# Kernel tuning notes

Hardware: AMD Instinct MI355X
Metric: run time of the kernel (lower is better)

## Reference

```python
import jax, jax.numpy as jnp
import numpy as np
from jax import lax

NUM_HEADS = 6
LN_EPS = 1e-5


def _ln(x, g, b):
    mu = jnp.mean(x, axis=-1, keepdims=True)
    var = jnp.mean(jnp.square(x - mu), axis=-1, keepdims=True)
    return (x - mu) * jax.lax.rsqrt(var + LN_EPS) * g + b


def _gelu(x):
    return jax.nn.gelu(x, approximate=False)


def setup_inputs() -> dict:
    key = jax.random.key(0)
    ks = jax.random.split(key, 16)
    B, N, C = 16, 1025, 384
    hid = 4 * C  # 1536
    k3 = 3  # depthwise kernel size
    s = 0.02
    rn = lambda k, shape: (jax.random.normal(k, shape, jnp.float32) * s)
    return {
        "x": jax.random.normal(ks[0], (B, N, C), jnp.float32),
        "ln1_g": jnp.ones((C,), jnp.float32),
        "ln1_b": jnp.zeros((C,), jnp.float32),
        "qkv_w": rn(ks[1], (3 * C, C)),
        "proj_w": rn(ks[2], (C, C)),
        "proj_b": jnp.zeros((C,), jnp.float32),
        "ln2_g": jnp.ones((C,), jnp.float32),
        "ln2_b": jnp.zeros((C,), jnp.float32),
        "conv1_w": rn(ks[3], (hid, C)),          # 1x1 conv as matrix
        "conv1_b": jnp.zeros((hid,), jnp.float32),
        "conv2_w": rn(ks[4], (hid, 1, k3, k3)),   # depthwise OIHW
        "conv2_b": jnp.zeros((hid,), jnp.float32),
        "conv3_w": rn(ks[5], (C, hid)),           # 1x1 conv as matrix
        "conv3_b": jnp.zeros((C,), jnp.float32),
        "bn1_s": jnp.ones((hid,), jnp.float32), "bn1_b": jnp.zeros((hid,), jnp.float32),
        "bn2_s": jnp.ones((hid,), jnp.float32), "bn2_b": jnp.zeros((hid,), jnp.float32),
        "bn3_s": jnp.ones((C,), jnp.float32), "bn3_b": jnp.zeros((C,), jnp.float32),
        "comp_w": rn(ks[6], (C // 4, C)), "comp_b": jnp.zeros((C // 4,), jnp.float32),
        "exc_w": rn(ks[7], (C, C // 4)), "exc_b": jnp.zeros((C,), jnp.float32),
    }


def _block(x, ln1_g, ln1_b, qkv_w, proj_w, proj_b, ln2_g, ln2_b,
           conv1_w, conv1_b, conv2_w, conv2_b, conv3_w, conv3_b,
           bn1_s, bn1_b, bn2_s, bn2_b, bn3_s, bn3_b,
           comp_w, comp_b, exc_w, exc_b):
    B, N, C = x.shape
    Hh = NUM_HEADS
    hd = C // Hh
    S = int(np.sqrt(N - 1))

    # ---- Attention (manual softmax(QK^T)V) ----
    h = _ln(x, ln1_g, ln1_b)
    qkv = jnp.einsum('bnc,dc->bnd', h, qkv_w).reshape(B, N, 3, Hh, hd)
    qkv = qkv.transpose(2, 0, 3, 1, 4)  # [3,B,H,N,hd]
    q, k, v = qkv[0], qkv[1], qkv[2]
    attn = jax.nn.softmax(jnp.einsum('bhqd,bhkd->bhqk', q, k) * (hd ** -0.5), axis=-1)
    o = jnp.einsum('bhqk,bhkd->bhqd', attn, v).transpose(0, 2, 1, 3).reshape(B, N, C)
    o = o @ proj_w.T + proj_b
    x = x + o

    # ---- DAFF FFN (conv + BN(eval affine) + GELU + SE gating on cls) ----
    h2 = _ln(x, ln2_g, ln2_b)
    cls_tok, tok = h2[:, :1], h2[:, 1:]
    t = tok.reshape(B, S, S, C).transpose(0, 3, 1, 2)  # NCHW
    hid = conv1_w.shape[0]
    y = jnp.einsum('bchw,oc->bohw', t, conv1_w) + conv1_b[None, :, None, None]
    y = y * bn1_s[None, :, None, None] + bn1_b[None, :, None, None]
    y = _gelu(y)
    shortcut = y
    y = lax.conv_general_dilated(y, conv2_w, (1, 1), 'SAME',
                                 feature_group_count=hid,
                                 dimension_numbers=('NCHW', 'OIHW', 'NCHW'))
    y = y + conv2_b[None, :, None, None]
    y = y * bn2_s[None, :, None, None] + bn2_b[None, :, None, None]
    y = shortcut + _gelu(y)
    y = jnp.einsum('bchw,oc->bohw', y, conv3_w) + conv3_b[None, :, None, None]
    y = y * bn3_s[None, :, None, None] + bn3_b[None, :, None, None]
    # SE gate on cls token
    w = jnp.mean(y, axis=(2, 3)).reshape(B, 1, C)
    w = _gelu(w @ comp_w.T + comp_b) @ exc_w.T + exc_b
    cls_out = cls_tok * w
    tok_out = y.reshape(B, C, S * S).transpose(0, 2, 1)
    out = jnp.concatenate([cls_out, tok_out], axis=1)
    return x + out


def reference(x, ln1_g, ln1_b, qkv_w, proj_w, proj_b, ln2_g, ln2_b,
              conv1_w, conv1_b, conv2_w, conv2_b, conv3_w, conv3_b,
              bn1_s, bn1_b, bn2_s, bn2_b, bn3_s, bn3_b,
              comp_w, comp_b, exc_w, exc_b):
    return _block(x, ln1_g, ln1_b, qkv_w, proj_w, proj_b, ln2_g, ln2_b,
                  conv1_w, conv1_b, conv2_w, conv2_b, conv3_w, conv3_b,
                  bn1_s, bn1_b, bn2_s, bn2_b, bn3_s, bn3_b,
                  comp_w, comp_b, exc_w, exc_b)
```

## Files before the change

kernel.cpp:

```cpp
#include <hip/hip_runtime.h>
#include <math.h>

#define DI __device__ __forceinline__

namespace {

constexpr int B_ = 16;
constexpr int N_ = 1025;
constexpr int C_ = 384;
constexpr int H_ = 6;
constexpr int HD_ = 64;
constexpr int HID_ = 1536;
constexpr int P_ = 1024;
constexpr int MTOK = B_ * P_;
constexpr int MALL = B_ * N_;
constexpr int NPAD = 1088;
constexpr long long AF = (long long)MALL * C_;

typedef __attribute__((ext_vector_type(4))) float f32x4;
typedef __attribute__((ext_vector_type(8))) short bf16x8;

DI float gelu_f(float x) { return 0.5f * x * (1.0f + erff(x * 0.7071067811865475f)); }

DI float us2f(unsigned short u) {
  union { unsigned int i; float f; } c; c.i = ((unsigned)u) << 16; return c.f;
}
DI unsigned short f2us(float f) {
  union { float f; unsigned int i; } c; c.f = f;
  unsigned int r = c.i + 0x7FFF + ((c.i >> 16) & 1);
  return (unsigned short)(r >> 16);
}
DI unsigned short f2us_trunc(float f) {
  union { float f; unsigned int i; } c; c.f = f;
  return (unsigned short)(c.i >> 16);
}
DI void bf8_to_f(const uint4 v, float* f) {
  const unsigned int u[4] = {v.x, v.y, v.z, v.w};
#pragma unroll
  for (int t = 0; t < 4; t++) {
    union { unsigned int i; float fl; } lo, hi;
    lo.i = (u[t] & 0xffffu) << 16;
    hi.i = u[t] & 0xffff0000u;
    f[2 * t] = lo.fl; f[2 * t + 1] = hi.fl;
  }
}
DI uint4 f_to_bf8(const float* f) {
  unsigned int w[4];
#pragma unroll
  for (int t = 0; t < 4; t++)
    w[t] = (unsigned)f2us(f[2 * t]) | ((unsigned)f2us(f[2 * t + 1]) << 16);
  return make_uint4(w[0], w[1], w[2], w[3]);
}

DI void gl2lds16(const unsigned short* g, unsigned short* l) {
  __builtin_amdgcn_global_load_lds(
      (const __attribute__((address_space(1))) void*)g,
      (__attribute__((address_space(3))) void*)l, 16, 0, 0);
}

__global__ __launch_bounds__(256) void cvt_kernel(const float* __restrict__ src,
                                                  unsigned short* __restrict__ dst, int n)
{
  const int i = blockIdx.x * 256 + threadIdx.x;
  if (i < n) dst[i] = f2us(src[i]);
}

__global__ __launch_bounds__(256) void wprep_kernel(
    const float* __restrict__ w2, const float* __restrict__ c2b,
    const float* __restrict__ s2, const float* __restrict__ b2,
    unsigned short* __restrict__ w2s, float* __restrict__ Bc)
{
  const int idx = blockIdx.x * 256 + threadIdx.x;
  if (idx < HID_ * 9) {
    const int tap = idx / HID_, c = idx % HID_;
    w2s[tap * HID_ + c] = f2us(w2[c * 9 + tap] * s2[c]);
  }
  if (idx < HID_) Bc[idx] = c2b[idx] * s2[idx] + b2[idx];
}

__global__ __launch_bounds__(128) void ln_kernel(
    const float* __restrict__ x, const float* __restrict__ g,
    const float* __restrict__ b, unsigned short* __restrict__ out,
    float* __restrict__ cls_out)
{
  const int row = blockIdx.x;
  const int t = threadIdx.x;
  const float* xr = x + (long long)row * C_;
  float v0 = xr[t], v1 = xr[t + 128], v2 = xr[t + 256];
  __shared__ float rs[128], rq[128];
  rs[t] = v0 + v1 + v2;
  rq[t] = v0 * v0 + v1 * v1 + v2 * v2;
  __syncthreads();
  for (int o = 64; o > 0; o >>= 1) {
    if (t < o) { rs[t] += rs[t + o]; rq[t] += rq[t + o]; }
    __syncthreads();
  }
  const float mean = rs[0] * (1.0f / C_);
  const float var  = rq[0] * (1.0f / C_) - mean * mean;
  const float rstd = rsqrtf(var + 1e-5f);
  unsigned short* orow = out + (long long)row * C_;
  const float r0 = (v0 - mean) * rstd * g[t]       + b[t];
  const float r1 = (v1 - mean) * rstd * g[t + 128] + b[t + 128];
  const float r2 = (v2 - mean) * rstd * g[t + 256] + b[t + 256];
  orow[t] = f2us(r0); orow[t + 128] = f2us(r1); orow[t + 256] = f2us(r2);
  if (cls_out != nullptr && (row % N_) == 0) {
    const int bb = row / N_;
    float* cr = cls_out + (long long)bb * C_;
    cr[t] = r0; cr[t + 128] = r1; cr[t + 256] = r2;
  }
}

__global__ __launch_bounds__(256) void vtrans_kernel(
    const unsigned short* __restrict__ v, unsigned short* __restrict__ vt)
{
  __shared__ unsigned short t[64][72];
  const int bh = blockIdx.x, nt = blockIdx.y;
  const int n0 = nt * 64;
  const int tid = threadIdx.x;
  {
    const int nl = tid >> 2;
    const int dc = (tid & 3) * 16;
    const int gn = n0 + nl;
    uint4 a = make_uint4(0u,0u,0u,0u), b = make_uint4(0u,0u,0u,0u);
    if (gn < N_) {
      const unsigned short* p = v + ((long long)bh * N_ + gn) * HD_ + dc;
      a = *(const uint4*)p; b = *(const uint4*)(p + 8);
    }
    *(uint4*)&t[nl][dc] = a;
    *(uint4*)&t[nl][dc + 8] = b;
  }
  __syncthreads();
  {
    const int dl = tid >> 2;
    const int nc = (tid & 3) * 16;
    unsigned short tmp[16];
#pragma unroll
    for (int i = 0; i < 16; i++) tmp[i] = t[nc + i][dl];
    unsigned short* p = vt + ((long long)bh * HD_ + dl) * NPAD + n0 + nc;
    *(uint4*)p = *(uint4*)&tmp[0];
    *(uint4*)(p + 8) = *(uint4*)&tmp[8];
  }
}

enum { GM_QKV = 0, GM_PROJ = 1, GM_CONV1 = 2, GM_CONV3 = 3 };

template <int MODE, int K>
__global__ __launch_bounds__(256) void mgemm_kernel(
    const unsigned short* __restrict__ A, const unsigned short* __restrict__ W,
    void* __restrict__ o0, void* __restrict__ o1, void* __restrict__ o2,
    const float* __restrict__ e0, const float* __restrict__ e1,
    const float* __restrict__ e2, int M)
{
  __shared__ unsigned short As[128][64];
  __shared__ unsigned short Bs[128][64];
  const int m0 = blockIdx.x * 128, n0 = blockIdx.y * 128;
  if (m0 >= M) return;
  const int tid = threadIdx.x;
  const int lane = tid & 63, wv = tid >> 6;
  const int lane15 = lane & 15, quad = lane >> 4;
  const int wm = (wv >> 1) * 64, wn = (wv & 1) * 64;

  const unsigned short* agp[4];
  const unsigned short* bgp[4];
#pragma unroll
  for (int t = 0; t < 4; t++) {
    const int lr = wv * 32 + t * 8 + (lane >> 3);
    const int chunk = (lane & 7) ^ (lr & 7);
    int gm = m0 + lr;
    if (gm > M - 1) gm = M - 1;
    long long arow = gm;
    if constexpr (MODE == GM_CONV1) arow = (long long)(gm >> 10) * N_ + 1 + (gm & 1023);
    agp[t] = A + arow * K + chunk * 8;
    bgp[t] = W + (long long)(n0 + lr) * K + chunk * 8;
  }

  f32x4 acc[4][4];
#pragma unroll
  for (int i = 0; i < 4; i++)
#pragma unroll
    for (int j = 0; j < 4; j++) acc[i][j] = (f32x4)0.f;

  const int xsel = lane15 & 7;
  for (int k0 = 0; k0 < K; k0 += 64) {
    __syncthreads();
#pragma unroll
    for (int t = 0; t < 4; t++) {
      gl2lds16(agp[t] + k0, &As[wv * 32 + t * 8][0]);
      gl2lds16(bgp[t] + k0, &Bs[wv * 32 + t * 8][0]);
    }
    __syncthreads();
#pragma unroll
    for (int kh = 0; kh < 2; kh++) {
      bf16x8 af[4], bfr[4];
#pragma unroll
      for (int i = 0; i < 4; i++)
        af[i] = *(const bf16x8*)&As[wm + i * 16 + lane15][((kh * 4 + quad) ^ xsel) * 8];
#pragma unroll
      for (int j = 0; j < 4; j++)
        bfr[j] = *(const bf16x8*)&Bs[wn + j * 16 + lane15][((kh * 4 + quad) ^ xsel) * 8];
#pragma unroll
      for (int i = 0; i < 4; i++)
#pragma unroll
        for (int j = 0; j < 4; j++)
          acc[i][j] = __builtin_amdgcn_mfma_f32_16x16x32_bf16(af[i], bfr[j], acc[i][j], 0, 0, 0);
    }
  }
#pragma unroll
  for (int i = 0; i < 4; i++) {
#pragma unroll
    for (int r = 0; r < 4; r++) {
      const int m = m0 + wm + i * 16 + quad * 4 + r;
      if (m >= M) continue;
#pragma unroll
      for (int j = 0; j < 4; j++) {
        const int n = n0 + wn + j * 16 + lane15;
        const float val = acc[i][j][r];
        if constexpr (MODE == GM_QKV) {
          const int which = n / C_, rr = n % C_, hh = rr >> 6, e = rr & 63;
          const int b = m / N_, nn = m % N_;
          unsigned short* dst = (unsigned short*)((which == 0) ? o0 : ((which == 1) ? o1 : o2));
          const float sval = (which == 0) ? val * 0.125f : val;
          dst[(((long long)b * H_ + hh) * N_ + nn) * HD_ + e] = f2us(sval);
        } else if constexpr (MODE == GM_PROJ) {
          ((float*)o0)[(long long)m * C_ + n] = val + e0[(long long)m * C_ + n] + e1[n];
        } else if constexpr (MODE == GM_CONV1) {
          ((unsigned short*)o0)[(long long)m * HID_ + n] =
              f2us(gelu_f((val + e0[n]) * e1[n] + e2[n]));
        } else {
          ((float*)o0)[(long long)m * C_ + n] = (val + e0[n]) * e1[n] + e2[n];
        }
      }
    }
  }
}

__global__ __launch_bounds__(256) void fattn_kernel(
    const unsigned short* __restrict__ q, const unsigned short* __restrict__ k,
    const unsigned short* __restrict__ vt, unsigned short* __restrict__ o)
{
  __shared__ unsigned short Ks[64][64];
  __shared__ unsigned short Vt[64][64];
  __shared__ unsigned short Ps[4][16][72];
  const int tid = threadIdx.x;
  const int lane = tid & 63, wv = tid >> 6;
  const int lane15 = lane & 15, quad = lane >> 4;
  const int bh = blockIdx.x, qt = blockIdx.y;
  const long long headoff = (long long)bh * N_;
  const int q0 = qt * 64 + wv * 16;

  const long long qrow = headoff + q0 + lane15;
  const bf16x8 aq0 = *(const bf16x8*)(q + qrow * HD_ + quad * 8);
  const bf16x8 aq1 = *(const bf16x8*)(q + qrow * HD_ + 32 + quad * 8);

  const unsigned short* kgp[2];
  const unsigned short* vgp[2];
#pragma unroll
  for (int t = 0; t < 2; t++) {
    const int row = wv * 16 + t * 8 + (lane >> 3);
    const int ch = (lane & 7) ^ (row & 7);
    kgp[t] = k + (headoff + row) * HD_ + ch * 8;
    vgp[t] = vt + ((long long)bh * HD_ + row) * NPAD + ch * 8;
  }

  f32x4 O[4];
  float l_r[4] = {0.f, 0.f, 0.f, 0.f};
#pragma unroll
  for (int n = 0; n < 4; n++) O[n] = (f32x4)0.f;

  const int xsel = lane15 & 7;
  for (int kt = 0; kt < 17; kt++) {
    const int kt0 = kt * 64;
    __syncthreads();
#pragma unroll
    for (int t = 0; t < 2; t++) {
      gl2lds16(kgp[t] + (long long)kt0 * HD_, &Ks[wv * 16 + t * 8][0]);
      gl2lds16(vgp[t] + kt0, &Vt[wv * 16 + t * 8][0]);
    }
    __syncthreads();

    f32x4 S[4];
#pragma unroll
    for (int n = 0; n < 4; n++) {
      S[n] = (f32x4)0.f;
      const bf16x8 b0 = *(const bf16x8*)&Ks[n * 16 + lane15][(quad ^ xsel) * 8];
      S[n] = __builtin_amdgcn_mfma_f32_16x16x32_bf16(aq0, b0, S[n], 0, 0, 0);
      const bf16x8 b1 = *(const bf16x8*)&Ks[n * 16 + lane15][((4 + quad) ^ xsel) * 8];
      S[n] = __builtin_amdgcn_mfma_f32_16x16x32_bf16(aq1, b1, S[n], 0, 0, 0);
    }
    if (kt == 16) {
#pragma unroll
      for (int n = 0; n < 4; n++) {
        if ((kt0 + n * 16 + lane15) >= N_)
#pragma unroll
          for (int r = 0; r < 4; r++) S[n][r] = -1e30f;
      }
    }
#pragma unroll
    for (int n = 0; n < 4; n++)
#pragma unroll
      for (int r = 0; r < 4; r++) {
        const float p = __expf(S[n][r]);
        l_r[r] += p;
        Ps[wv][quad * 4 + r][n * 16 + lane15] = f2us_trunc(p);
      }
#pragma unroll
    for (int half = 0; half < 2; half++) {
      const bf16x8 ap = *(const bf16x8*)&Ps[wv][lane15][half * 32 + quad * 8];
#pragma unroll
      for (int n = 0; n < 4; n++) {
        const bf16x8 bv =
            *(const bf16x8*)&Vt[n * 16 + lane15][(((half * 4 + quad)) ^ xsel) * 8];
        O[n] = __builtin_amdgcn_mfma_f32_16x16x32_bf16(ap, bv, O[n], 0, 0, 0);
      }
    }
  }
#pragma unroll
  for (int msk = 1; msk < 16; msk <<= 1)
#pragma unroll
    for (int r = 0; r < 4; r++) l_r[r] += __shfl_xor(l_r[r], msk, 64);

  const int b = bh / H_, hh = bh % H_;
#pragma unroll
  for (int r = 0; r < 4; r++) {
    const int gq = q0 + quad * 4 + r;
    if (gq < N_) {
      const float inv = 1.0f / l_r[r];
#pragma unroll
      for (int n = 0; n < 4; n++)
        o[((long long)b * N_ + gq) * C_ + hh * HD_ + n * 16 + lane15] = f2us(O[n][r] * inv);
    }
  }
}

__global__ __launch_bounds__(192) void dwconv_kernel(
    const unsigned short* __restrict__ y1, const unsigned short* __restrict__ w2s,
    const float* __restrict__ Bc, unsigned short* __restrict__ y2)
{
  const int p = blockIdx.x & 1023;
  const int b = blockIdx.x >> 10;
  const int i = p >> 5, j = p & 31;
  const int cb = threadIdx.x << 3;
  const long long tokbase = (long long)blockIdx.x * HID_;
  float acc[8] = {};
#pragma unroll
  for (int di = -1; di <= 1; di++) {
    const int ii = i + di;
    if (ii < 0 || ii > 31) continue;
#pragma unroll
    for (int dj = -1; dj <= 1; dj++) {
      const int jj = j + dj;
      if (jj < 0 || jj > 31) continue;
      const int tap = (di + 1) * 3 + (dj + 1);
      const uint4 dv = *(const uint4*)(y1 + ((long long)b * P_ + ii * 32 + jj) * HID_ + cb);
      const uint4 wv = *(const uint4*)(w2s + tap * HID_ + cb);
      float df[8], wf[8];
      bf8_to_f(dv, df); bf8_to_f(wv, wf);
#pragma unroll
      for (int t = 0; t < 8; t++) acc[t] += df[t] * wf[t];
    }
  }
  const uint4 sv = *(const uint4*)(y1 + tokbase + cb);
  float sf[8]; bf8_to_f(sv, sf);
  const float4 bc0 = *(const float4*)(Bc + cb);
  const float4 bc1 = *(const float4*)(Bc + cb + 4);
  const float bcv[8] = {bc0.x, bc0.y, bc0.z, bc0.w, bc1.x, bc1.y, bc1.z, bc1.w};
  float of[8];
#pragma unroll
  for (int t = 0; t < 8; t++) of[t] = sf[t] + gelu_f(acc[t] + bcv[t]);
  *(uint4*)(y2 + tokbase + cb) = f_to_bf8(of);
}

__global__ __launch_bounds__(384) void pool_kernel(const float* __restrict__ y3,
                                                   float* __restrict__ w0p)
{
  const int b = blockIdx.x, chunk = blockIdx.y;
  const int c = threadIdx.x;
  float s = 0.f;
  for (int p = chunk * 64; p < chunk * 64 + 64; p++)
    s += y3[((long long)b * P_ + p) * C_ + c];
  w0p[((long long)b * 16 + chunk) * C_ + c] = s;
}

__global__ __launch_bounds__(128) void se_kernel(
    const float* __restrict__ w0p, const float* __restrict__ cw,
    const float* __restrict__ cb, const float* __restrict__ ew,
    const float* __restrict__ eb, float* __restrict__ wfin)
{
  __shared__ float wm[384];
  __shared__ float t1[96];
  const int b = blockIdx.x, t = threadIdx.x;
  for (int c = t; c < 384; c += 128) {
    float s = 0.f;
    for (int ch = 0; ch < 16; ch++) s += w0p[((long long)b * 16 + ch) * C_ + c];
    wm[c] = s * (1.0f / 1024.0f);
  }
  __syncthreads();
  if (t < 96) {
    float s = cb[t];
    for (int c = 0; c < 384; c++) s += wm[c] * cw[t * 384 + c];
    t1[t] = gelu_f(s);
  }
  __syncthreads();
  for (int c = t; c < 384; c += 128) {
    float s = eb[c];
    for (int j = 0; j < 96; j++) s += t1[j] * ew[c * 96 + j];
    wfin[(long long)b * C_ + c] = s;
  }
}

__global__ __launch_bounds__(256) void assemble_kernel(
    const float* __restrict__ x2, const float* __restrict__ cls,
    const float* __restrict__ y3, const float* __restrict__ wfin,
    float* __restrict__ out)
{
  const long long idx = (long long)blockIdx.x * 256 + threadIdx.x;
  if (idx >= AF) return;
  const int c = (int)(idx % C_);
  const long long row = idx / C_;
  const int b = (int)(row / N_);
  const int n = (int)(row % N_);
  float add;
  if (n == 0) add = cls[(long long)b * C_ + c] * wfin[(long long)b * C_ + c];
  else        add = y3[((long long)b * P_ + n - 1) * C_ + c];
  out[idx] = x2[idx] + add;
}

}

extern "C" void kernel_launch(void* const* d_in, const int* in_sizes, int n_in,
                              void* d_out, int out_size, void* d_ws, size_t ws_size,
                              hipStream_t stream)
{
  const float* x       = (const float*)d_in[0];
  const float* ln1_g   = (const float*)d_in[1];
  const float* ln1_b   = (const float*)d_in[2];
  const float* qkv_w   = (const float*)d_in[3];
  const float* proj_w  = (const float*)d_in[4];
  const float* proj_b  = (const float*)d_in[5];
  const float* ln2_g   = (const float*)d_in[6];
  const float* ln2_b   = (const float*)d_in[7];
  const float* conv1_w = (const float*)d_in[8];
  const float* conv1_b = (const float*)d_in[9];
  const float* conv2_w = (const float*)d_in[10];
  const float* conv2_b = (const float*)d_in[11];
  const float* conv3_w = (const float*)d_in[12];
  const float* conv3_b = (const float*)d_in[13];
  const float* bn1_s   = (const float*)d_in[14];
  const float* bn1_b   = (const float*)d_in[15];
  const float* bn2_s   = (const float*)d_in[16];
  const float* bn2_b   = (const float*)d_in[17];
  const float* bn3_s   = (const float*)d_in[18];
  const float* bn3_b   = (const float*)d_in[19];
  const float* comp_w  = (const float*)d_in[20];
  const float* comp_b  = (const float*)d_in[21];
  const float* exc_w   = (const float*)d_in[22];
  const float* exc_b   = (const float*)d_in[23];

  char* wsb = (char*)d_ws;
  const size_t RA = 50331648, RB = 50331648, RC = 25190400;
  const int NQKV = 3 * C_ * C_;
  const int NPROJ = C_ * C_;
  const int NC1 = HID_ * C_;
  const int NC3 = C_ * HID_;
  const int NW2 = HID_ * 9;
  const size_t tailbytes = (size_t)(NQKV + NPROJ + NC1 + NC3 + NW2) * 2 +
                           (size_t)(HID_ + B_ * C_ + B_ * 16 * C_ + B_ * C_) * 4;
  const size_t needed = RA + RB + RC + tailbytes;
  if (ws_size < needed) return;

  unsigned short* qb  = (unsigned short*)wsb;
  unsigned short* kb  = qb + AF;
  unsigned short* vb  = kb + AF;
  unsigned short* h2b = (unsigned short*)wsb;
  unsigned short* y2  = (unsigned short*)wsb;
  char* rb = wsb + RA;
  unsigned short* hb  = (unsigned short*)rb;
  unsigned short* o16 = (unsigned short*)rb;
  unsigned short* y1  = (unsigned short*)rb;
  float* y3           = (float*)rb;
  unsigned short* vtb = (unsigned short*)(wsb + RA + RB);
  float* x2 = (float*)(wsb + RA + RB);
  unsigned short* wqkv16 = (unsigned short*)(wsb + RA + RB + RC);
  unsigned short* wproj16 = wqkv16 + NQKV;
  unsigned short* wc116 = wproj16 + NPROJ;
  unsigned short* wc316 = wc116 + NC1;
  unsigned short* w2s  = wc316 + NC3;
  float* Bc   = (float*)(w2s + NW2);
  float* cls  = Bc + HID_;
  float* w0p  = cls + B_ * C_;
  float* wfin = w0p + B_ * 16 * C_;

  cvt_kernel<<<(NQKV + 255) / 256, 256, 0, stream>>>(qkv_w, wqkv16, NQKV);
  cvt_kernel<<<(NPROJ + 255) / 256, 256, 0, stream>>>(proj_w, wproj16, NPROJ);
  cvt_kernel<<<(NC1 + 255) / 256, 256, 0, stream>>>(conv1_w, wc116, NC1);
  cvt_kernel<<<(NC3 + 255) / 256, 256, 0, stream>>>(conv3_w, wc316, NC3);
  wprep_kernel<<<(NW2 + 255) / 256, 256, 0, stream>>>(conv2_w, conv2_b, bn2_s, bn2_b, w2s, Bc);
  ln_kernel<<<MALL, 128, 0, stream>>>(x, ln1_g, ln1_b, hb, nullptr);
  mgemm_kernel<GM_QKV, 384><<<dim3(136, 9), 256, 0, stream>>>(
      hb, wqkv16, qb, kb, vb, nullptr, nullptr, nullptr, MALL);
  vtrans_kernel<<<dim3(B_ * H_, 17), 256, 0, stream>>>(vb, vtb);
  fattn_kernel<<<dim3(B_ * H_, 17), 256, 0, stream>>>(qb, kb, vtb, o16);
  mgemm_kernel<GM_PROJ, 384><<<dim3(136, 3), 256, 0, stream>>>(
      o16, wproj16, x2, nullptr, nullptr, x, proj_b, nullptr, MALL);
  ln_kernel<<<MALL, 128, 0, stream>>>(x2, ln2_g, ln2_b, h2b, cls);
  mgemm_kernel<GM_CONV1, 384><<<dim3(128, 12), 256, 0, stream>>>(
      h2b, wc116, y1, nullptr, nullptr, conv1_b, bn1_s, bn1_b, MTOK);
  dwconv_kernel<<<MTOK, 192, 0, stream>>>(y1, w2s, Bc, y2);
  mgemm_kernel<GM_CONV3, 1536><<<dim3(128, 3), 256, 0, stream>>>(
      y2, wc316, y3, nullptr, nullptr, conv3_b, bn3_s, bn3_b, MTOK);
  pool_kernel<<<dim3(B_, 16), 384, 0, stream>>>(y3, w0p);
  se_kernel<<<B_, 128, 0, stream>>>(w0p, comp_w, comp_b, exc_w, exc_b, wfin);
  assemble_kernel<<<(int)((AF + 255) / 256), 256, 0, stream>>>(x2, cls, y3, wfin, (float*)d_out);
}
```

Baseline: 442.5 us.

## Fuse residual into conv3 epilogue, warp-level LN, exp2 softmax, 2-token dwconv

Merges weight conversion kernels into one launch and rewrites LayerNorm to use one wavefront per row with shuffle reductions. Folds log2(e) into the Q scale so attention can use exp2. Processes two adjacent tokens per depthwise-conv block to reuse loaded columns and weights. Moves the final residual add into the conv3 GEMM epilogue, leaving only a small cls-row fix kernel, which removes a full-tensor pass at the cost of scattered epilogue writes.

```diff
diff --git a/kernel.cpp b/kernel.cpp
--- a/kernel.cpp
+++ b/kernel.cpp
@@ -17,6 +17,14 @@
 constexpr int NPAD = 1088;
 constexpr long long AF = (long long)MALL * C_;
 
+constexpr int NQKV = 3 * C_ * C_;
+constexpr int NPROJ = C_ * C_;
+constexpr int NC1 = HID_ * C_;
+constexpr int NC3 = C_ * HID_;
+constexpr int NW2 = HID_ * 9;
+constexpr int T1 = NQKV, T2 = T1 + NPROJ, T3 = T2 + NC1, T4 = T3 + NC3;
+constexpr int T5 = T4 + NW2, T6 = T5 + HID_;
+
 typedef __attribute__((ext_vector_type(4))) float f32x4;
 typedef __attribute__((ext_vector_type(8))) short bf16x8;
 
@@ -58,55 +66,59 @@
       (__attribute__((address_space(3))) void*)l, 16, 0, 0);
 }
 
-__global__ __launch_bounds__(256) void cvt_kernel(const float* __restrict__ src,
-                                                  unsigned short* __restrict__ dst, int n)
-{
-  const int i = blockIdx.x * 256 + threadIdx.x;
-  if (i < n) dst[i] = f2us(src[i]);
-}
-
-__global__ __launch_bounds__(256) void wprep_kernel(
-    const float* __restrict__ w2, const float* __restrict__ c2b,
+__global__ __launch_bounds__(256) void cvtall_kernel(
+    const float* __restrict__ qkv_w, const float* __restrict__ proj_w,
+    const float* __restrict__ conv1_w, const float* __restrict__ conv3_w,
+    const float* __restrict__ conv2_w, const float* __restrict__ c2b,
     const float* __restrict__ s2, const float* __restrict__ b2,
-    unsigned short* __restrict__ w2s, float* __restrict__ Bc)
+    unsigned short* __restrict__ dst16, float* __restrict__ Bc)
 {
   const int idx = blockIdx.x * 256 + threadIdx.x;
-  if (idx < HID_ * 9) {
-    const int tap = idx / HID_, c = idx % HID_;
-    w2s[tap * HID_ + c] = f2us(w2[c * 9 + tap] * s2[c]);
-  }
-  if (idx < HID_) Bc[idx] = c2b[idx] * s2[idx] + b2[idx];
-}
-
-__global__ __launch_bounds__(128) void ln_kernel(
+  if (idx < T1)      dst16[idx] = f2us(qkv_w[idx]);
+  else if (idx < T2) dst16[idx] = f2us(proj_w[idx - T1]);
+  else if (idx < T3) dst16[idx] = f2us(conv1_w[idx - T2]);
+  else if (idx < T4) dst16[idx] = f2us(conv3_w[idx - T3]);
+  else if (idx < T5) {
+    const int r = idx - T4, tap = r / HID_, c = r % HID_;
+    dst16[idx] = f2us(conv2_w[c * 9 + tap] * s2[c]);
+  } else if (idx < T6) {
+    const int c = idx - T5;
+    Bc[c] = c2b[c] * s2[c] + b2[c];
+  }
+}
+
+__global__ __launch_bounds__(256) void lnw_kernel(
     const float* __restrict__ x, const float* __restrict__ g,
     const float* __restrict__ b, unsigned short* __restrict__ out,
-    float* __restrict__ cls_out)
-{
-  const int row = blockIdx.x;
-  const int t = threadIdx.x;
+    float* __restrict__ cls_out, int nrows)
+{
+  const int row = blockIdx.x * 4 + (threadIdx.x >> 6);
+  if (row >= nrows) return;
+  const int lane = threadIdx.x & 63;
   const float* xr = x + (long long)row * C_;
-  float v0 = xr[t], v1 = xr[t + 128], v2 = xr[t + 256];
-  __shared__ float rs[128], rq[128];
-  rs[t] = v0 + v1 + v2;
-  rq[t] = v0 * v0 + v1 * v1 + v2 * v2;
-  __syncthreads();
-  for (int o = 64; o > 0; o >>= 1) {
-    if (t < o) { rs[t] += rs[t + o]; rq[t] += rq[t + o]; }
-    __syncthreads();
-  }
-  const float mean = rs[0] * (1.0f / C_);
-  const float var  = rq[0] * (1.0f / C_) - mean * mean;
+  float v[6];
+#pragma unroll
+  for (int i = 0; i < 6; i++) v[i] = xr[lane + 64 * i];
+  float s = 0.f, q = 0.f;
+#pragma unroll
+  for (int i = 0; i < 6; i++) { s += v[i]; q += v[i] * v[i]; }
+#pragma unroll
+  for (int m = 1; m < 64; m <<= 1) {
+    s += __shfl_xor(s, m, 64);
+    q += __shfl_xor(q, m, 64);
+  }
+  const float mean = s * (1.0f / C_);
+  const float var  = q * (1.0f / C_) - mean * mean;
   const float rstd = rsqrtf(var + 1e-5f);
   unsigned short* orow = out + (long long)row * C_;
-  const float r0 = (v0 - mean) * rstd * g[t]       + b[t];
-  const float r1 = (v1 - mean) * rstd * g[t + 128] + b[t + 128];
-  const float r2 = (v2 - mean) * rstd * g[t + 256] + b[t + 256];
-  orow[t] = f2us(r0); orow[t + 128] = f2us(r1); orow[t + 256] = f2us(r2);
-  if (cls_out != nullptr && (row % N_) == 0) {
-    const int bb = row / N_;
-    float* cr = cls_out + (long long)bb * C_;
-    cr[t] = r0; cr[t + 128] = r1; cr[t + 256] = r2;
+  const bool iscls = (cls_out != nullptr) && (row % N_) == 0;
+  float* cr = iscls ? cls_out + (long long)(row / N_) * C_ : nullptr;
+#pragma unroll
+  for (int i = 0; i < 6; i++) {
+    const int c = lane + 64 * i;
+    const float r = (v[i] - mean) * rstd * g[c] + b[c];
+    orow[c] = f2us(r);
+    if (iscls) cr[c] = r;
   }
 }
 
@@ -219,7 +231,7 @@
           const int which = n / C_, rr = n % C_, hh = rr >> 6, e = rr & 63;
           const int b = m / N_, nn = m % N_;
           unsigned short* dst = (unsigned short*)((which == 0) ? o0 : ((which == 1) ? o1 : o2));
-          const float sval = (which == 0) ? val * 0.125f : val;
+          const float sval = (which == 0) ? val * 0.18033688f : val;
           dst[(((long long)b * H_ + hh) * N_ + nn) * HD_ + e] = f2us(sval);
         } else if constexpr (MODE == GM_PROJ) {
           ((float*)o0)[(long long)m * C_ + n] = val + e0[(long long)m * C_ + n] + e1[n];
@@ -227,7 +239,11 @@
           ((unsigned short*)o0)[(long long)m * HID_ + n] =
               f2us(gelu_f((val + e0[n]) * e1[n] + e2[n]));
         } else {
-          ((float*)o0)[(long long)m * C_ + n] = (val + e0[n]) * e1[n] + e2[n];
+          const float val2 = (val + e0[n]) * e1[n] + e2[n];
+          ((float*)o0)[(long long)m * C_ + n] = val2;
+          const int bb = m >> 10, pp = m & 1023;
+          const long long orow = ((long long)bb * N_ + 1 + pp) * C_ + n;
+          ((float*)o1)[orow] = ((const float*)o2)[orow] + val2;
         }
       }
     }
@@ -299,7 +315,7 @@
     for (int n = 0; n < 4; n++)
 #pragma unroll
       for (int r = 0; r < 4; r++) {
-        const float p = __expf(S[n][r]);
+        const float p = exp2f(S[n][r]);
         l_r[r] += p;
         Ps[wv][quad * 4 + r][n * 16 + lane15] = f2us_trunc(p);
       }
@@ -336,38 +352,63 @@
     const unsigned short* __restrict__ y1, const unsigned short* __restrict__ w2s,
     const float* __restrict__ Bc, unsigned short* __restrict__ y2)
 {
-  const int p = blockIdx.x & 1023;
-  const int b = blockIdx.x >> 10;
-  const int i = p >> 5, j = p & 31;
+  const int jp = blockIdx.x & 15;
+  const int i  = (blockIdx.x >> 4) & 31;
+  const int b  = blockIdx.x >> 9;
+  const int j0 = jp * 2;
   const int cb = threadIdx.x << 3;
-  const long long tokbase = (long long)blockIdx.x * HID_;
-  float acc[8] = {};
+
+  float wf[9][8];
+#pragma unroll
+  for (int tap = 0; tap < 9; tap++) {
+    const uint4 wv = *(const uint4*)(w2s + tap * HID_ + cb);
+    bf8_to_f(wv, wf[tap]);
+  }
+  float acc0[8] = {}, acc1[8] = {};
+  float sh0[8], sh1[8];
 #pragma unroll
   for (int di = -1; di <= 1; di++) {
     const int ii = i + di;
     if (ii < 0 || ii > 31) continue;
-#pragma unroll
-    for (int dj = -1; dj <= 1; dj++) {
-      const int jj = j + dj;
+    const long long rowbase = ((long long)b * P_ + ii * 32) * HID_ + cb;
+#pragma unroll
+    for (int dj = -1; dj <= 2; dj++) {
+      const int jj = j0 + dj;
       if (jj < 0 || jj > 31) continue;
-      const int tap = (di + 1) * 3 + (dj + 1);
-      const uint4 dv = *(const uint4*)(y1 + ((long long)b * P_ + ii * 32 + jj) * HID_ + cb);
-      const uint4 wv = *(const uint4*)(w2s + tap * HID_ + cb);
-      float df[8], wf[8];
-      bf8_to_f(dv, df); bf8_to_f(wv, wf);
-#pragma unroll
-      for (int t = 0; t < 8; t++) acc[t] += df[t] * wf[t];
-    }
-  }
-  const uint4 sv = *(const uint4*)(y1 + tokbase + cb);
-  float sf[8]; bf8_to_f(sv, sf);
+      const uint4 dv = *(const uint4*)(y1 + rowbase + (long long)jj * HID_);
+      float df[8]; bf8_to_f(dv, df);
+      if (dj <= 1) {
+        const int tap = (di + 1) * 3 + (dj + 1);
+#pragma unroll
+        for (int t = 0; t < 8; t++) acc0[t] += df[t] * wf[tap][t];
+      }
+      if (dj >= 0) {
+        const int tap = (di + 1) * 3 + dj;
+#pragma unroll
+        for (int t = 0; t < 8; t++) acc1[t] += df[t] * wf[tap][t];
+      }
+      if (di == 0 && dj == 0) {
+#pragma unroll
+        for (int t = 0; t < 8; t++) sh0[t] = df[t];
+      }
+      if (di == 0 && dj == 1) {
+#pragma unroll
+        for (int t = 0; t < 8; t++) sh1[t] = df[t];
+      }
+    }
+  }
   const float4 bc0 = *(const float4*)(Bc + cb);
   const float4 bc1 = *(const float4*)(Bc + cb + 4);
   const float bcv[8] = {bc0.x, bc0.y, bc0.z, bc0.w, bc1.x, bc1.y, bc1.z, bc1.w};
-  float of[8];
-#pragma unroll
-  for (int t = 0; t < 8; t++) of[t] = sf[t] + gelu_f(acc[t] + bcv[t]);
-  *(uint4*)(y2 + tokbase + cb) = f_to_bf8(of);
+  float of0[8], of1[8];
+#pragma unroll
+  for (int t = 0; t < 8; t++) {
+    of0[t] = sh0[t] + gelu_f(acc0[t] + bcv[t]);
+    of1[t] = sh1[t] + gelu_f(acc1[t] + bcv[t]);
+  }
+  const long long tok0 = ((long long)b * P_ + i * 32 + j0) * HID_ + cb;
+  *(uint4*)(y2 + tok0) = f_to_bf8(of0);
+  *(uint4*)(y2 + tok0 + HID_) = f_to_bf8(of1);
 }
 
 __global__ __launch_bounds__(384) void pool_kernel(const float* __restrict__ y3,
@@ -408,21 +449,15 @@
   }
 }
 
-__global__ __launch_bounds__(256) void assemble_kernel(
+__global__ __launch_bounds__(256) void clsfix_kernel(
     const float* __restrict__ x2, const float* __restrict__ cls,
-    const float* __restrict__ y3, const float* __restrict__ wfin,
-    float* __restrict__ out)
-{
-  const long long idx = (long long)blockIdx.x * 256 + threadIdx.x;
-  if (idx >= AF) return;
-  const int c = (int)(idx % C_);
-  const long long row = idx / C_;
-  const int b = (int)(row / N_);
-  const int n = (int)(row % N_);
-  float add;
-  if (n == 0) add = cls[(long long)b * C_ + c] * wfin[(long long)b * C_ + c];
-  else        add = y3[((long long)b * P_ + n - 1) * C_ + c];
-  out[idx] = x2[idx] + add;
+    const float* __restrict__ wfin, float* __restrict__ out)
+{
+  const int idx = blockIdx.x * 256 + threadIdx.x;
+  if (idx >= B_ * C_) return;
+  const int b = idx / C_, c = idx % C_;
+  const long long row = (long long)b * N_ * C_ + c;
+  out[row] = x2[row] + cls[idx] * wfin[idx];
 }
 
 }
@@ -458,12 +493,7 @@
 
   char* wsb = (char*)d_ws;
   const size_t RA = 50331648, RB = 50331648, RC = 25190400;
-  const int NQKV = 3 * C_ * C_;
-  const int NPROJ = C_ * C_;
-  const int NC1 = HID_ * C_;
-  const int NC3 = C_ * HID_;
-  const int NW2 = HID_ * 9;
-  const size_t tailbytes = (size_t)(NQKV + NPROJ + NC1 + NC3 + NW2) * 2 +
+  const size_t tailbytes = (size_t)T5 * 2 +
                            (size_t)(HID_ + B_ * C_ + B_ * 16 * C_ + B_ * C_) * 4;
   const size_t needed = RA + RB + RC + tailbytes;
   if (ws_size < needed) return;
@@ -480,35 +510,33 @@
   float* y3           = (float*)rb;
   unsigned short* vtb = (unsigned short*)(wsb + RA + RB);
   float* x2 = (float*)(wsb + RA + RB);
-  unsigned short* wqkv16 = (unsigned short*)(wsb + RA + RB + RC);
-  unsigned short* wproj16 = wqkv16 + NQKV;
-  unsigned short* wc116 = wproj16 + NPROJ;
-  unsigned short* wc316 = wc116 + NC1;
-  unsigned short* w2s  = wc316 + NC3;
-  float* Bc   = (float*)(w2s + NW2);
+  unsigned short* w16 = (unsigned short*)(wsb + RA + RB + RC);
+  unsigned short* wqkv16  = w16;
+  unsigned short* wproj16 = w16 + T1;
+  unsigned short* wc116   = w16 + T2;
+  unsigned short* wc316   = w16 + T3;
+  unsigned short* w2s     = w16 + T4;
+  float* Bc   = (float*)(w16 + T5);
   float* cls  = Bc + HID_;
   float* w0p  = cls + B_ * C_;
   float* wfin = w0p + B_ * 16 * C_;
 
-  cvt_kernel<<<(NQKV + 255) / 256, 256, 0, stream>>>(qkv_w, wqkv16, NQKV);
-  cvt_kernel<<<(NPROJ + 255) / 256, 256, 0, stream>>>(proj_w, wproj16, NPROJ);
-  cvt_kernel<<<(NC1 + 255) / 256, 256, 0, stream>>>(conv1_w, wc116, NC1);
-  cvt_kernel<<<(NC3 + 255) / 256, 256, 0, stream>>>(conv3_w, wc316, NC3);
-  wprep_kernel<<<(NW2 + 255) / 256, 256, 0, stream>>>(conv2_w, conv2_b, bn2_s, bn2_b, w2s, Bc);
-  ln_kernel<<<MALL, 128, 0, stream>>>(x, ln1_g, ln1_b, hb, nullptr);
+  cvtall_kernel<<<(T6 + 255) / 256, 256, 0, stream>>>(
+      qkv_w, proj_w, conv1_w, conv3_w, conv2_w, conv2_b, bn2_s, bn2_b, w16, Bc);
+  lnw_kernel<<<(MALL + 3) / 4, 256, 0, stream>>>(x, ln1_g, ln1_b, hb, nullptr, MALL);
   mgemm_kernel<GM_QKV, 384><<<dim3(136, 9), 256, 0, stream>>>(
       hb, wqkv16, qb, kb, vb, nullptr, nullptr, nullptr, MALL);
   vtrans_kernel<<<dim3(B_ * H_, 17), 256, 0, stream>>>(vb, vtb);
   fattn_kernel<<<dim3(B_ * H_, 17), 256, 0, stream>>>(qb, kb, vtb, o16);
   mgemm_kernel<GM_PROJ, 384><<<dim3(136, 3), 256, 0, stream>>>(
       o16, wproj16, x2, nullptr, nullptr, x, proj_b, nullptr, MALL);
-  ln_kernel<<<MALL, 128, 0, stream>>>(x2, ln2_g, ln2_b, h2b, cls);
+  lnw_kernel<<<(MALL + 3) / 4, 256, 0, stream>>>(x2, ln2_g, ln2_b, h2b, cls, MALL);
   mgemm_kernel<GM_CONV1, 384><<<dim3(128, 12), 256, 0, stream>>>(
       h2b, wc116, y1, nullptr, nullptr, conv1_b, bn1_s, bn1_b, MTOK);
-  dwconv_kernel<<<MTOK, 192, 0, stream>>>(y1, w2s, Bc, y2);
+  dwconv_kernel<<<B_ * 32 * 16, 192, 0, stream>>>(y1, w2s, Bc, y2);
   mgemm_kernel<GM_CONV3, 1536><<<dim3(128, 3), 256, 0, stream>>>(
-      y2, wc316, y3, nullptr, nullptr, conv3_b, bn3_s, bn3_b, MTOK);
+      y2, wc316, y3, (float*)d_out, x2, conv3_b, bn3_s, bn3_b, MTOK);
   pool_kernel<<<dim3(B_, 16), 384, 0, stream>>>(y3, w0p);
   se_kernel<<<B_, 128, 0, stream>>>(w0p, comp_w, comp_b, exc_w, exc_b, wfin);
-  assemble_kernel<<<(int)((AF + 255) / 256), 256, 0, stream>>>(x2, cls, y3, wfin, (float*)d_out);
-}
+  clsfix_kernel<<<(B_ * C_ + 255) / 256, 256, 0, stream>>>(x2, cls, wfin, (float*)d_out);
+}
```

After: 422.6 us. 4.5% less time.
